# Kernel optimization log

Measured on AMD Instinct MI355X. Metric: run time of the kernel, lower is better.

Reference implementation:

```python
import jax, jax.numpy as jnp
import numpy as np

EMBED_DIM = 1024
NUM_HEADS = 16
HEAD_DIM = EMBED_DIM // NUM_HEADS
T, B = 2048, 2


def setup_inputs() -> dict:
    key = jax.random.key(0)
    ks = jax.random.split(key, 12)
    s = 1.0 / np.sqrt(EMBED_DIM)
    x = jax.random.normal(ks[0], (T, B, EMBED_DIM), dtype=jnp.float32)
    time_decay = jax.random.uniform(ks[1], (T, B, 1), dtype=jnp.float32)
    # causal mask: masked_fill where mask == 0
    attn_mask = jnp.tril(jnp.ones((T, T), dtype=jnp.int32))
    Wq = jax.random.uniform(ks[2], (EMBED_DIM, EMBED_DIM), jnp.float32, -s, s)
    bq = jax.random.uniform(ks[3], (EMBED_DIM,), jnp.float32, -s, s)
    Wk = jax.random.uniform(ks[4], (EMBED_DIM, EMBED_DIM), jnp.float32, -s, s)
    bk = jax.random.uniform(ks[5], (EMBED_DIM,), jnp.float32, -s, s)
    Wv = jax.random.uniform(ks[6], (EMBED_DIM, EMBED_DIM), jnp.float32, -s, s)
    bv = jax.random.uniform(ks[7], (EMBED_DIM,), jnp.float32, -s, s)
    Wo = jax.random.uniform(ks[8], (EMBED_DIM, EMBED_DIM), jnp.float32, -s, s)
    bo = jax.random.uniform(ks[9], (EMBED_DIM,), jnp.float32, -s, s)
    return {"x": x, "time_decay": time_decay, "attn_mask": attn_mask,
            "Wq": Wq, "bq": bq, "Wk": Wk, "bk": bk,
            "Wv": Wv, "bv": bv, "Wo": Wo, "bo": bo}


def reference(x, time_decay, attn_mask, Wq, bq, Wk, bk, Wv, bv, Wo, bo):
    t, b, e = x.shape
    h, d = NUM_HEADS, HEAD_DIM
    # linear (torch: y = x @ W.T + b), then split heads -> (B, H, T, D)
    def proj(W, bias):
        y = jnp.einsum('tbe,fe->tbf', x, W) + bias
        return y.reshape(t, b, h, d).transpose(1, 2, 0, 3)
    Q, K, V = proj(Wq, bq), proj(Wk, bk), proj(Wv, bv)
    scores = jnp.einsum('bhqd,bhkd->bhqk', Q, K) / np.sqrt(d).astype(jnp.float32)
    scores = jnp.where(attn_mask == 0, jnp.float32(-1e9), scores)
    attn = jax.nn.softmax(scores, axis=-1)
    out = jnp.einsum('bhqk,bhkd->bhqd', attn, V)      # (B,H,T,D)
    out = out.transpose(2, 0, 1, 3).reshape(t, b, e)   # (T,B,E)
    out = jnp.einsum('tbe,fe->tbf', out, Wo) + bo
    return out * time_decay
```

## Files before the change

kernel.cpp:

```cpp
#include <hip/hip_runtime.h>


typedef unsigned short u16;
typedef __attribute__((ext_vector_type(8))) short bf16x8_t;
typedef __attribute__((ext_vector_type(4))) float fx4_t;

#define T_SEQ 2048
#define BATCH 2
#define EMB   1024
#define NH    16
#define HD    64
#define MROWS (T_SEQ * BATCH)

#define EXP2F(x) __builtin_amdgcn_exp2f(x)

__device__ __forceinline__ float bf2f(u16 u) {
  union { unsigned int i; float f; } v;
  v.i = ((unsigned int)u) << 16;
  return v.f;
}
__device__ __forceinline__ u16 f2bf(float f) {
  union { float f; unsigned int i; } v;
  v.f = f;
  unsigned int x = v.i;
  unsigned int r = (x + 0x7fffu + ((x >> 16) & 1u)) >> 16;
  return (u16)r;
}

__global__ void cvt_all(const float* __restrict__ x,
                        const float* __restrict__ wq, const float* __restrict__ wk,
                        const float* __restrict__ wv, const float* __restrict__ wo,
                        u16* __restrict__ xb,
                        u16* __restrict__ wqb, u16* __restrict__ wkb,
                        u16* __restrict__ wvb, u16* __restrict__ wob) {
  int i = blockIdx.x * blockDim.x + threadIdx.x;
  const float* src; u16* dst; int off;
  if (i < 1048576)      { src = x;  dst = xb;  off = i; }
  else if (i < 1310720) { src = wq; dst = wqb; off = i - 1048576; }
  else if (i < 1572864) { src = wk; dst = wkb; off = i - 1310720; }
  else if (i < 1835008) { src = wv; dst = wvb; off = i - 1572864; }
  else                  { src = wo; dst = wob; off = i - 1835008; }
  float4 v = ((const float4*)src)[off];
  ushort4 o;
  o.x = f2bf(v.x); o.y = f2bf(v.y); o.z = f2bf(v.z); o.w = f2bf(v.w);
  ((ushort4*)dst)[off] = o;
}

__global__ __launch_bounds__(256, 2) void gemm_qkv(
    const u16* __restrict__ xb,
    const u16* __restrict__ wq, const u16* __restrict__ wk, const u16* __restrict__ wv,
    const float* __restrict__ bq, const float* __restrict__ bk, const float* __restrict__ bv,
    u16* __restrict__ Qh, u16* __restrict__ Kh, u16* __restrict__ VTg) {
  __shared__ short As[128 * 72];
  __shared__ short Bs[128 * 72];

  const int z = blockIdx.z;
  const u16* W = (z == 0) ? wq : (z == 1) ? wk : wv;
  const float* bias = (z == 0) ? bq : (z == 1) ? bk : bv;
  u16* dst = (z == 0) ? Qh : (z == 1) ? Kh : VTg;

  const int tid = threadIdx.x;
  const int bm = blockIdx.x, bn = blockIdx.y;
  const int lane = tid & 63, wv_id = tid >> 6;
  const int wm = wv_id >> 1, wn = wv_id & 1;
  const int lr = lane & 15, quad = lane >> 4;

  fx4_t acc[4][4];
#pragma unroll
  for (int i = 0; i < 4; i++)
#pragma unroll
    for (int j = 0; j < 4; j++) acc[i][j] = (fx4_t){0.f, 0.f, 0.f, 0.f};

  for (int k0 = 0; k0 < EMB; k0 += 64) {
#pragma unroll
    for (int it = 0; it < 4; ++it) {
      int g = tid + it * 256;
      int r = g >> 3, c = g & 7;
      const int4* sa = (const int4*)(xb + (size_t)(bm * 128 + r) * EMB + k0 + c * 8);
      *(int4*)&As[r * 72 + c * 8] = *sa;
      const int4* sb = (const int4*)(W + (size_t)(bn * 128 + r) * EMB + k0 + c * 8);
      *(int4*)&Bs[r * 72 + c * 8] = *sb;
    }
    __syncthreads();
#pragma unroll
    for (int ks = 0; ks < 2; ++ks) {
      bf16x8_t a[4], b[4];
      const int goff = (ks * 4 + quad) * 8;
#pragma unroll
      for (int i = 0; i < 4; i++) a[i] = *(const bf16x8_t*)&As[(wm * 64 + i * 16 + lr) * 72 + goff];
#pragma unroll
      for (int j = 0; j < 4; j++) b[j] = *(const bf16x8_t*)&Bs[(wn * 64 + j * 16 + lr) * 72 + goff];
#pragma unroll
      for (int i = 0; i < 4; i++)
#pragma unroll
        for (int j = 0; j < 4; j++)
          acc[i][j] = __builtin_amdgcn_mfma_f32_16x16x32_bf16(a[i], b[j], acc[i][j], 0, 0, 0);
    }
    __syncthreads();
  }

#pragma unroll
  for (int i = 0; i < 4; i++) {
#pragma unroll
    for (int j = 0; j < 4; j++) {
      const int n = bn * 128 + wn * 64 + j * 16 + lr;
      const float bsv = bias[n];
      const int h = n >> 6, d = n & 63;
#pragma unroll
      for (int r = 0; r < 4; r++) {
        const int m = bm * 128 + wm * 64 + i * 16 + quad * 4 + r;
        const int t = m >> 1, bb = m & 1;
        float v = acc[i][j][r] + bsv;
        if (z == 2) {
          dst[((size_t)(bb * NH + h) * HD + d) * T_SEQ + t] = f2bf(v);
        } else {
          dst[((size_t)(bb * NH + h) * T_SEQ + t) * HD + d] = f2bf(v);
        }
      }
    }
  }
}

__global__ __launch_bounds__(256, 2) void gemm_out(
    const u16* __restrict__ Ob, const u16* __restrict__ wo,
    const float* __restrict__ bo, const float* __restrict__ td,
    float* __restrict__ out) {
  __shared__ short As[128 * 72];
  __shared__ short Bs[128 * 72];

  const int tid = threadIdx.x;
  const int bm = blockIdx.x, bn = blockIdx.y;
  const int lane = tid & 63, wv_id = tid >> 6;
  const int wm = wv_id >> 1, wn = wv_id & 1;
  const int lr = lane & 15, quad = lane >> 4;

  fx4_t acc[4][4];
#pragma unroll
  for (int i = 0; i < 4; i++)
#pragma unroll
    for (int j = 0; j < 4; j++) acc[i][j] = (fx4_t){0.f, 0.f, 0.f, 0.f};

  for (int k0 = 0; k0 < EMB; k0 += 64) {
#pragma unroll
    for (int it = 0; it < 4; ++it) {
      int g = tid + it * 256;
      int r = g >> 3, c = g & 7;
      const int4* sa = (const int4*)(Ob + (size_t)(bm * 128 + r) * EMB + k0 + c * 8);
      *(int4*)&As[r * 72 + c * 8] = *sa;
      const int4* sb = (const int4*)(wo + (size_t)(bn * 128 + r) * EMB + k0 + c * 8);
      *(int4*)&Bs[r * 72 + c * 8] = *sb;
    }
    __syncthreads();
#pragma unroll
    for (int ks = 0; ks < 2; ++ks) {
      bf16x8_t a[4], b[4];
      const int goff = (ks * 4 + quad) * 8;
#pragma unroll
      for (int i = 0; i < 4; i++) a[i] = *(const bf16x8_t*)&As[(wm * 64 + i * 16 + lr) * 72 + goff];
#pragma unroll
      for (int j = 0; j < 4; j++) b[j] = *(const bf16x8_t*)&Bs[(wn * 64 + j * 16 + lr) * 72 + goff];
#pragma unroll
      for (int i = 0; i < 4; i++)
#pragma unroll
        for (int j = 0; j < 4; j++)
          acc[i][j] = __builtin_amdgcn_mfma_f32_16x16x32_bf16(a[i], b[j], acc[i][j], 0, 0, 0);
    }
    __syncthreads();
  }

#pragma unroll
  for (int i = 0; i < 4; i++) {
#pragma unroll
    for (int j = 0; j < 4; j++) {
      const int n = bn * 128 + wn * 64 + j * 16 + lr;
      const float bsv = bo[n];
#pragma unroll
      for (int r = 0; r < 4; r++) {
        const int m = bm * 128 + wm * 64 + i * 16 + quad * 4 + r;
        float v = (acc[i][j][r] + bsv) * td[m];
        out[(size_t)m * EMB + n] = v;
      }
    }
  }
}

__global__ __launch_bounds__(256, 4) void attn_mfma2(
    const u16* __restrict__ Qh, const u16* __restrict__ Kh, const u16* __restrict__ VTg,
    u16* __restrict__ Ob) {
  __shared__ short Ks[64 * 72];
  __shared__ short Vt[64 * 72];
  __shared__ short Ps[4][16 * 72];

  const int blk = blockIdx.x;
  const int bh = blk & 31;
  const int j = blk >> 5;
  const int qt = (j & 1) ? (31 - (j >> 1)) : (j >> 1);
  const int qb = qt * 64;

  const int tid = threadIdx.x;
  const int w = tid >> 6, lane = tid & 63;
  const int lr = lane & 15, quad = lane >> 4;

  const u16* Qb = Qh + (size_t)bh * T_SEQ * HD;
  const u16* Kb = Kh + (size_t)bh * T_SEQ * HD;
  const u16* VTb = VTg + (size_t)bh * HD * T_SEQ;

  const float QSCALE = 0.18033688f;
  bf16x8_t qf[2];
#pragma unroll
  for (int ks = 0; ks < 2; ks++) {
    bf16x8_t v = *(const bf16x8_t*)(Qb + (size_t)(qb + w * 16 + lr) * HD + ks * 32 + quad * 8);
    bf16x8_t o;
#pragma unroll
    for (int e = 0; e < 8; e++) o[e] = (short)f2bf(bf2f((u16)v[e]) * QSCALE);
    qf[ks] = o;
  }

  fx4_t acc_o[4];
#pragma unroll
  for (int dn = 0; dn < 4; dn++) acc_o[dn] = (fx4_t){0.f, 0.f, 0.f, 0.f};
  float m_i = -1e30f, l_i = 0.f;

  const int nkt = qt + 1;
  for (int kt = 0; kt < nkt; kt++) {
    const int k0 = kt * 64;
    __syncthreads();

#pragma unroll
    for (int it = 0; it < 2; it++) {
      int g = tid + it * 256;
      int r = g >> 3, c8 = (g & 7) * 8;
      *(int4*)&Ks[r * 72 + c8] = *(const int4*)(Kb + (size_t)(k0 + r) * HD + c8);
      *(int4*)&Vt[r * 72 + c8] = *(const int4*)(VTb + (size_t)r * T_SEQ + k0 + c8);
    }
    __syncthreads();

    fx4_t st[4];
#pragma unroll
    for (int nt = 0; nt < 4; nt++) st[nt] = (fx4_t){0.f, 0.f, 0.f, 0.f};
#pragma unroll
    for (int ks = 0; ks < 2; ks++) {
#pragma unroll
      for (int nt = 0; nt < 4; nt++) {
        bf16x8_t kf = *(const bf16x8_t*)&Ks[(nt * 16 + lr) * 72 + ks * 32 + quad * 8];
        st[nt] = __builtin_amdgcn_mfma_f32_16x16x32_bf16(kf, qf[ks], st[nt], 0, 0, 0);
      }
    }

    if (kt == qt) {
#pragma unroll
      for (int nt = 0; nt < 4; nt++)
#pragma unroll
        for (int r = 0; r < 4; r++)
          if (nt * 16 + quad * 4 + r > w * 16 + lr) st[nt][r] = -1e30f;
    }

    float rmax = -1e30f;
#pragma unroll
    for (int nt = 0; nt < 4; nt++)
#pragma unroll
      for (int r = 0; r < 4; r++) rmax = fmaxf(rmax, st[nt][r]);
    rmax = fmaxf(rmax, __shfl_xor(rmax, 16));
    rmax = fmaxf(rmax, __shfl_xor(rmax, 32));
    const float mn = fmaxf(m_i, rmax);
    const float alpha = EXP2F(m_i - mn);
    m_i = mn;
    float rsum = 0.f;
#pragma unroll
    for (int nt = 0; nt < 4; nt++) {
#pragma unroll
      for (int r = 0; r < 4; r++) {
        float e = EXP2F(st[nt][r] - mn);
        st[nt][r] = e;
        rsum += e;
      }
    }
    rsum += __shfl_xor(rsum, 16);
    rsum += __shfl_xor(rsum, 32);
    l_i = l_i * alpha + rsum;

    short* Pw = Ps[w];
#pragma unroll
    for (int nt = 0; nt < 4; nt++) {
      short4 pv;
      pv.x = (short)f2bf(st[nt][0]);
      pv.y = (short)f2bf(st[nt][1]);
      pv.z = (short)f2bf(st[nt][2]);
      pv.w = (short)f2bf(st[nt][3]);
      *(short4*)&Pw[lr * 72 + nt * 16 + quad * 4] = pv;
    }

#pragma unroll
    for (int r = 0; r < 4; r++) {
      const float a_r = __shfl(alpha, quad * 4 + r);
#pragma unroll
      for (int dn = 0; dn < 4; dn++) acc_o[dn][r] *= a_r;
    }

#pragma unroll
    for (int ks = 0; ks < 2; ks++) {
      bf16x8_t pf = *(const bf16x8_t*)&Pw[lr * 72 + ks * 32 + quad * 8];
#pragma unroll
      for (int dn = 0; dn < 4; dn++) {
        bf16x8_t vf = *(const bf16x8_t*)&Vt[(dn * 16 + lr) * 72 + ks * 32 + quad * 8];
        acc_o[dn] = __builtin_amdgcn_mfma_f32_16x16x32_bf16(pf, vf, acc_o[dn], 0, 0, 0);
      }
    }
  }

  const float inv = 1.0f / l_i;
  const int b = bh >> 4, h = bh & 15;
#pragma unroll
  for (int r = 0; r < 4; r++) {
    const float inv_r = __shfl(inv, quad * 4 + r);
    const int t = qb + w * 16 + quad * 4 + r;
#pragma unroll
    for (int dn = 0; dn < 4; dn++) {
      const int d = dn * 16 + lr;
      Ob[(size_t)(t * BATCH + b) * EMB + h * HD + d] = f2bf(acc_o[dn][r] * inv_r);
    }
  }
}

extern "C" void kernel_launch(void* const* d_in, const int* in_sizes, int n_in,
                              void* d_out, int out_size, void* d_ws, size_t ws_size,
                              hipStream_t stream) {
  const float* x  = (const float*)d_in[0];
  const float* td = (const float*)d_in[1];
  const float* Wq = (const float*)d_in[3];
  const float* bq = (const float*)d_in[4];
  const float* Wk = (const float*)d_in[5];
  const float* bk = (const float*)d_in[6];
  const float* Wv = (const float*)d_in[7];
  const float* bv = (const float*)d_in[8];
  const float* Wo = (const float*)d_in[9];
  const float* bo = (const float*)d_in[10];
  float* out = (float*)d_out;

  char* ws = (char*)d_ws;
  u16* xb  = (u16*)(ws + 0);
  u16* wqb = (u16*)(ws + ((size_t)8  << 20));
  u16* wkb = (u16*)(ws + ((size_t)10 << 20));
  u16* wvb = (u16*)(ws + ((size_t)12 << 20));
  u16* wob = (u16*)(ws + ((size_t)14 << 20));
  u16* Qh  = (u16*)(ws + ((size_t)16 << 20));
  u16* Kh  = (u16*)(ws + ((size_t)24 << 20));
  u16* VTg = (u16*)(ws + ((size_t)32 << 20));
  u16* Ob  = xb;

  cvt_all<<<8192, 256, 0, stream>>>(x, Wq, Wk, Wv, Wo, xb, wqb, wkb, wvb, wob);

  gemm_qkv<<<dim3(MROWS / 128, EMB / 128, 3), 256, 0, stream>>>(
      xb, wqb, wkb, wvb, bq, bk, bv, Qh, Kh, VTg);

  attn_mfma2<<<1024, 256, 0, stream>>>(Qh, Kh, VTg, Ob);

  gemm_out<<<dim3(MROWS / 128, EMB / 128), 256, 0, stream>>>(Ob, wob, bo, td, out);
}
```

Baseline: 222.8 us.

## Use direct global-to-LDS loads, double-buffer attention K/V, shrink output GEMM tile

Replaces the register-staged global-to-shared copies in all three compute kernels with global_load_lds direct loads into unpadded 64-wide LDS tiles. The attention kernel now double-buffers K and V tiles, so the next tile is prefetched while the current one is computed, with one barrier per iteration. The output GEMM uses 64-row M tiles to launch more blocks. The unpadded LDS layout may raise bank conflicts on the MFMA fragment reads, and attention occupancy drops to 3 blocks per CU in the launch bounds.

```diff
diff --git a/kernel.cpp b/kernel.cpp
--- a/kernel.cpp
+++ b/kernel.cpp
@@ -25,6 +25,12 @@
   unsigned int x = v.i;
   unsigned int r = (x + 0x7fffu + ((x >> 16) & 1u)) >> 16;
   return (u16)r;
+}
+
+__device__ __forceinline__ void glds16(const void* g, void* l) {
+  __builtin_amdgcn_global_load_lds(
+      (const __attribute__((address_space(1))) unsigned int*)g,
+      (__attribute__((address_space(3))) unsigned int*)l, 16, 0, 0);
 }
 
 __global__ void cvt_all(const float* __restrict__ x,
@@ -51,19 +57,19 @@
     const u16* __restrict__ wq, const u16* __restrict__ wk, const u16* __restrict__ wv,
     const float* __restrict__ bq, const float* __restrict__ bk, const float* __restrict__ bv,
     u16* __restrict__ Qh, u16* __restrict__ Kh, u16* __restrict__ VTg) {
-  __shared__ short As[128 * 72];
-  __shared__ short Bs[128 * 72];
+  __shared__ short As[128 * 64];
+  __shared__ short Bs[128 * 64];
 
   const int z = blockIdx.z;
   const u16* W = (z == 0) ? wq : (z == 1) ? wk : wv;
   const float* bias = (z == 0) ? bq : (z == 1) ? bk : bv;
-  u16* dst = (z == 0) ? Qh : (z == 1) ? Kh : VTg;
 
   const int tid = threadIdx.x;
   const int bm = blockIdx.x, bn = blockIdx.y;
-  const int lane = tid & 63, wv_id = tid >> 6;
-  const int wm = wv_id >> 1, wn = wv_id & 1;
+  const int lane = tid & 63, w = tid >> 6;
+  const int wm = w >> 1, wn = w & 1;
   const int lr = lane & 15, quad = lane >> 4;
+  const int r0 = lane >> 3, c8 = (lane & 7) * 8;
 
   fx4_t acc[4][4];
 #pragma unroll
@@ -73,13 +79,10 @@
 
   for (int k0 = 0; k0 < EMB; k0 += 64) {
 #pragma unroll
-    for (int it = 0; it < 4; ++it) {
-      int g = tid + it * 256;
-      int r = g >> 3, c = g & 7;
-      const int4* sa = (const int4*)(xb + (size_t)(bm * 128 + r) * EMB + k0 + c * 8);
-      *(int4*)&As[r * 72 + c * 8] = *sa;
-      const int4* sb = (const int4*)(W + (size_t)(bn * 128 + r) * EMB + k0 + c * 8);
-      *(int4*)&Bs[r * 72 + c * 8] = *sb;
+    for (int i = 0; i < 4; i++) {
+      const int rr = w * 32 + i * 8;
+      glds16(xb + (size_t)(bm * 128 + rr + r0) * EMB + k0 + c8, &As[rr * 64]);
+      glds16(W  + (size_t)(bn * 128 + rr + r0) * EMB + k0 + c8, &Bs[rr * 64]);
     }
     __syncthreads();
 #pragma unroll
@@ -87,9 +90,9 @@
       bf16x8_t a[4], b[4];
       const int goff = (ks * 4 + quad) * 8;
 #pragma unroll
-      for (int i = 0; i < 4; i++) a[i] = *(const bf16x8_t*)&As[(wm * 64 + i * 16 + lr) * 72 + goff];
-#pragma unroll
-      for (int j = 0; j < 4; j++) b[j] = *(const bf16x8_t*)&Bs[(wn * 64 + j * 16 + lr) * 72 + goff];
+      for (int i = 0; i < 4; i++) a[i] = *(const bf16x8_t*)&As[(wm * 64 + i * 16 + lr) * 64 + goff];
+#pragma unroll
+      for (int j = 0; j < 4; j++) b[j] = *(const bf16x8_t*)&Bs[(wn * 64 + j * 16 + lr) * 64 + goff];
 #pragma unroll
       for (int i = 0; i < 4; i++)
 #pragma unroll
@@ -112,8 +115,9 @@
         const int t = m >> 1, bb = m & 1;
         float v = acc[i][j][r] + bsv;
         if (z == 2) {
-          dst[((size_t)(bb * NH + h) * HD + d) * T_SEQ + t] = f2bf(v);
+          VTg[((size_t)(bb * NH + h) * HD + d) * T_SEQ + t] = f2bf(v);
         } else {
+          u16* dst = (z == 0) ? Qh : Kh;
           dst[((size_t)(bb * NH + h) * T_SEQ + t) * HD + d] = f2bf(v);
         }
       }
@@ -125,42 +129,44 @@
     const u16* __restrict__ Ob, const u16* __restrict__ wo,
     const float* __restrict__ bo, const float* __restrict__ td,
     float* __restrict__ out) {
-  __shared__ short As[128 * 72];
-  __shared__ short Bs[128 * 72];
+  __shared__ short As[64 * 64];
+  __shared__ short Bs[128 * 64];
 
   const int tid = threadIdx.x;
   const int bm = blockIdx.x, bn = blockIdx.y;
-  const int lane = tid & 63, wv_id = tid >> 6;
-  const int wm = wv_id >> 1, wn = wv_id & 1;
+  const int lane = tid & 63, w = tid >> 6;
+  const int wm = w >> 1, wn = w & 1;
   const int lr = lane & 15, quad = lane >> 4;
-
-  fx4_t acc[4][4];
-#pragma unroll
-  for (int i = 0; i < 4; i++)
+  const int r0 = lane >> 3, c8 = (lane & 7) * 8;
+
+  fx4_t acc[2][4];
+#pragma unroll
+  for (int i = 0; i < 2; i++)
 #pragma unroll
     for (int j = 0; j < 4; j++) acc[i][j] = (fx4_t){0.f, 0.f, 0.f, 0.f};
 
   for (int k0 = 0; k0 < EMB; k0 += 64) {
 #pragma unroll
-    for (int it = 0; it < 4; ++it) {
-      int g = tid + it * 256;
-      int r = g >> 3, c = g & 7;
-      const int4* sa = (const int4*)(Ob + (size_t)(bm * 128 + r) * EMB + k0 + c * 8);
-      *(int4*)&As[r * 72 + c * 8] = *sa;
-      const int4* sb = (const int4*)(wo + (size_t)(bn * 128 + r) * EMB + k0 + c * 8);
-      *(int4*)&Bs[r * 72 + c * 8] = *sb;
+    for (int i = 0; i < 2; i++) {
+      const int rr = w * 16 + i * 8;
+      glds16(Ob + (size_t)(bm * 64 + rr + r0) * EMB + k0 + c8, &As[rr * 64]);
+    }
+#pragma unroll
+    for (int i = 0; i < 4; i++) {
+      const int rr = w * 32 + i * 8;
+      glds16(wo + (size_t)(bn * 128 + rr + r0) * EMB + k0 + c8, &Bs[rr * 64]);
     }
     __syncthreads();
 #pragma unroll
     for (int ks = 0; ks < 2; ++ks) {
-      bf16x8_t a[4], b[4];
+      bf16x8_t a[2], b[4];
       const int goff = (ks * 4 + quad) * 8;
 #pragma unroll
-      for (int i = 0; i < 4; i++) a[i] = *(const bf16x8_t*)&As[(wm * 64 + i * 16 + lr) * 72 + goff];
-#pragma unroll
-      for (int j = 0; j < 4; j++) b[j] = *(const bf16x8_t*)&Bs[(wn * 64 + j * 16 + lr) * 72 + goff];
-#pragma unroll
-      for (int i = 0; i < 4; i++)
+      for (int i = 0; i < 2; i++) a[i] = *(const bf16x8_t*)&As[(wm * 32 + i * 16 + lr) * 64 + goff];
+#pragma unroll
+      for (int j = 0; j < 4; j++) b[j] = *(const bf16x8_t*)&Bs[(wn * 64 + j * 16 + lr) * 64 + goff];
+#pragma unroll
+      for (int i = 0; i < 2; i++)
 #pragma unroll
         for (int j = 0; j < 4; j++)
           acc[i][j] = __builtin_amdgcn_mfma_f32_16x16x32_bf16(a[i], b[j], acc[i][j], 0, 0, 0);
@@ -169,26 +175,25 @@
   }
 
 #pragma unroll
-  for (int i = 0; i < 4; i++) {
+  for (int i = 0; i < 2; i++) {
 #pragma unroll
     for (int j = 0; j < 4; j++) {
       const int n = bn * 128 + wn * 64 + j * 16 + lr;
       const float bsv = bo[n];
 #pragma unroll
       for (int r = 0; r < 4; r++) {
-        const int m = bm * 128 + wm * 64 + i * 16 + quad * 4 + r;
-        float v = (acc[i][j][r] + bsv) * td[m];
-        out[(size_t)m * EMB + n] = v;
-      }
-    }
-  }
-}
-
-__global__ __launch_bounds__(256, 4) void attn_mfma2(
+        const int m = bm * 64 + wm * 32 + i * 16 + quad * 4 + r;
+        out[(size_t)m * EMB + n] = (acc[i][j][r] + bsv) * td[m];
+      }
+    }
+  }
+}
+
+__global__ __launch_bounds__(256, 3) void attn_mfma3(
     const u16* __restrict__ Qh, const u16* __restrict__ Kh, const u16* __restrict__ VTg,
     u16* __restrict__ Ob) {
-  __shared__ short Ks[64 * 72];
-  __shared__ short Vt[64 * 72];
+  __shared__ short Kd[2][64 * 64];
+  __shared__ short Vd[2][64 * 64];
   __shared__ short Ps[4][16 * 72];
 
   const int blk = blockIdx.x;
@@ -200,6 +205,7 @@
   const int tid = threadIdx.x;
   const int w = tid >> 6, lane = tid & 63;
   const int lr = lane & 15, quad = lane >> 4;
+  const int r0 = lane >> 3, c8 = (lane & 7) * 8;
 
   const u16* Qb = Qh + (size_t)bh * T_SEQ * HD;
   const u16* Kb = Kh + (size_t)bh * T_SEQ * HD;
@@ -221,19 +227,24 @@
   for (int dn = 0; dn < 4; dn++) acc_o[dn] = (fx4_t){0.f, 0.f, 0.f, 0.f};
   float m_i = -1e30f, l_i = 0.f;
 
+#define STAGE(kt_, buf_)                                                          \
+  {                                                                               \
+    const int k0_ = (kt_) * 64;                                                   \
+    _Pragma("unroll")                                                             \
+    for (int i = 0; i < 2; i++) {                                                 \
+      const int rr = w * 16 + i * 8;                                              \
+      glds16(Kb + (size_t)(k0_ + rr + r0) * HD + c8, &Kd[buf_][rr * 64]);         \
+      glds16(VTb + (size_t)(rr + r0) * T_SEQ + k0_ + c8, &Vd[buf_][rr * 64]);     \
+    }                                                                             \
+  }
+
   const int nkt = qt + 1;
+  STAGE(0, 0);
+  __syncthreads();
+
   for (int kt = 0; kt < nkt; kt++) {
-    const int k0 = kt * 64;
-    __syncthreads();
-
-#pragma unroll
-    for (int it = 0; it < 2; it++) {
-      int g = tid + it * 256;
-      int r = g >> 3, c8 = (g & 7) * 8;
-      *(int4*)&Ks[r * 72 + c8] = *(const int4*)(Kb + (size_t)(k0 + r) * HD + c8);
-      *(int4*)&Vt[r * 72 + c8] = *(const int4*)(VTb + (size_t)r * T_SEQ + k0 + c8);
-    }
-    __syncthreads();
+    const int buf = kt & 1;
+    if (kt + 1 < nkt) STAGE(kt + 1, buf ^ 1);
 
     fx4_t st[4];
 #pragma unroll
@@ -242,7 +253,7 @@
     for (int ks = 0; ks < 2; ks++) {
 #pragma unroll
       for (int nt = 0; nt < 4; nt++) {
-        bf16x8_t kf = *(const bf16x8_t*)&Ks[(nt * 16 + lr) * 72 + ks * 32 + quad * 8];
+        bf16x8_t kf = *(const bf16x8_t*)&Kd[buf][(nt * 16 + lr) * 64 + ks * 32 + quad * 8];
         st[nt] = __builtin_amdgcn_mfma_f32_16x16x32_bf16(kf, qf[ks], st[nt], 0, 0, 0);
       }
     }
@@ -302,11 +313,14 @@
       bf16x8_t pf = *(const bf16x8_t*)&Pw[lr * 72 + ks * 32 + quad * 8];
 #pragma unroll
       for (int dn = 0; dn < 4; dn++) {
-        bf16x8_t vf = *(const bf16x8_t*)&Vt[(dn * 16 + lr) * 72 + ks * 32 + quad * 8];
+        bf16x8_t vf = *(const bf16x8_t*)&Vd[buf][(dn * 16 + lr) * 64 + ks * 32 + quad * 8];
         acc_o[dn] = __builtin_amdgcn_mfma_f32_16x16x32_bf16(pf, vf, acc_o[dn], 0, 0, 0);
       }
     }
-  }
+
+    __syncthreads();
+  }
+#undef STAGE
 
   const float inv = 1.0f / l_i;
   const int b = bh >> 4, h = bh & 15;
@@ -353,7 +367,7 @@
   gemm_qkv<<<dim3(MROWS / 128, EMB / 128, 3), 256, 0, stream>>>(
       xb, wqb, wkb, wvb, bq, bk, bv, Qh, Kh, VTg);
 
-  attn_mfma2<<<1024, 256, 0, stream>>>(Qh, Kh, VTg, Ob);
-
-  gemm_out<<<dim3(MROWS / 128, EMB / 128), 256, 0, stream>>>(Ob, wob, bo, td, out);
-}
+  attn_mfma3<<<1024, 256, 0, stream>>>(Qh, Kh, VTg, Ob);
+
+  gemm_out<<<dim3(MROWS / 64, EMB / 128), 256, 0, stream>>>(Ob, wob, bo, td, out);
+}
```

Result: slower. 229.8 us (+3.1%).
